# Performance work log

Hardware: AMD Instinct MI355X
Metric: run time of the kernel (lower is better)

The kernel has to match this reference:

```python
import jax, jax.numpy as jnp
import numpy as np

N = 2097152
RES = 512
N_LEVELS = 6  # 512,256,128,64,32,16 (stop at LIGHT_MIN_RES=16)
MIN_ROUGHNESS = 0.08
MAX_ROUGHNESS = 0.5


def _dot(a, b):
    return jnp.sum(a * b, axis=-1, keepdims=True)


def _safe_normalize(x):
    return x / jnp.sqrt(jnp.clip(_dot(x, x), 1e-20, None))


def _reflect(x, n):
    return 2.0 * _dot(x, n) * n - x


def _rgb_to_srgb(x):
    return jnp.where(x <= 0.0031308, 12.92 * x,
                     1.055 * jnp.power(jnp.maximum(x, 0.0031308), 1.0 / 2.4) - 0.055)


def _cube_face_uv(d):
    # OpenGL / nvdiffrast cube-map convention (inverse of util.cube_to_dir)
    x, y, z = d[..., 0], d[..., 1], d[..., 2]
    ax, ay, az = jnp.abs(x), jnp.abs(y), jnp.abs(z)
    is_x = (ax >= ay) & (ax >= az)
    is_y = (~is_x) & (ay >= az)
    face = jnp.where(is_x, jnp.where(x > 0, 0, 1),
           jnp.where(is_y, jnp.where(y > 0, 2, 3),
                           jnp.where(z > 0, 4, 5)))
    ma = jnp.maximum(jnp.where(is_x, ax, jnp.where(is_y, ay, az)), 1e-20)
    u = jnp.where(is_x, jnp.where(x > 0, -z, z),
        jnp.where(is_y, x, jnp.where(z > 0, x, -x)))
    v = jnp.where(is_y, jnp.where(y > 0, z, -z), -y)
    return face, u / ma, v / ma


def _bilinear_gather(tex, face, fx, fy):
    # tex: [6,H,W,C]; face/fx/fy: [N]
    H, W = tex.shape[1], tex.shape[2]
    x0 = jnp.floor(fx); y0 = jnp.floor(fy)
    tx = (fx - x0)[:, None]; ty = (fy - y0)[:, None]
    x0i = jnp.clip(x0.astype(jnp.int32), 0, W - 1)
    x1i = jnp.clip(x0i + 1, 0, W - 1)
    y0i = jnp.clip(y0.astype(jnp.int32), 0, H - 1)
    y1i = jnp.clip(y0i + 1, 0, H - 1)
    c00 = tex[face, y0i, x0i]; c01 = tex[face, y0i, x1i]
    c10 = tex[face, y1i, x0i]; c11 = tex[face, y1i, x1i]
    return (c00 * (1 - tx) + c01 * tx) * (1 - ty) + (c10 * (1 - tx) + c11 * tx) * ty


def _sample_cubemap(tex, dirs):
    H, W = tex.shape[1], tex.shape[2]
    face, u, v = _cube_face_uv(dirs)
    return _bilinear_gather(tex, face, (u * 0.5 + 0.5) * W - 0.5, (v * 0.5 + 0.5) * H - 0.5)


def _sample_cubemap_mip(mips, dirs, level):
    # trilinear: bilinear in each of the two bracketing mip levels + lerp on level
    L = len(mips)
    samples = jnp.stack([_sample_cubemap(m, dirs) for m in mips], axis=0)  # [L,N,C]
    lvl = jnp.clip(level, 0.0, L - 1.0)
    l0 = jnp.floor(lvl).astype(jnp.int32)
    l1 = jnp.minimum(l0 + 1, L - 1)
    f = (lvl - l0.astype(lvl.dtype))[:, None]
    n = jnp.arange(dirs.shape[0])
    return samples[l0, n] * (1 - f) + samples[l1, n] * f


def _sample_lut(lut, uv):
    # lut: [H,W,C]; uv in [0,1], u -> width, v -> height, clamp boundary
    H, W = lut.shape[0], lut.shape[1]
    fx = uv[:, 0] * W - 0.5; fy = uv[:, 1] * H - 0.5
    x0 = jnp.floor(fx); y0 = jnp.floor(fy)
    tx = (fx - x0)[:, None]; ty = (fy - y0)[:, None]
    x0i = jnp.clip(x0.astype(jnp.int32), 0, W - 1); x1i = jnp.clip(x0i + 1, 0, W - 1)
    y0i = jnp.clip(y0.astype(jnp.int32), 0, H - 1); y1i = jnp.clip(y0i + 1, 0, H - 1)
    c00 = lut[y0i, x0i]; c01 = lut[y0i, x1i]; c10 = lut[y1i, x0i]; c11 = lut[y1i, x1i]
    return (c00 * (1 - tx) + c01 * tx) * (1 - ty) + (c10 * (1 - tx) + c11 * tx) * ty


def _get_mip(roughness, n_levels):
    lo = (jnp.clip(roughness, MIN_ROUGHNESS, MAX_ROUGHNESS) - MIN_ROUGHNESS) \
         / (MAX_ROUGHNESS - MIN_ROUGHNESS) * (n_levels - 2)
    hi = (jnp.clip(roughness, MAX_ROUGHNESS, 1.0) - MAX_ROUGHNESS) / (1.0 - MAX_ROUGHNESS) + n_levels - 2
    return jnp.where(roughness < MAX_ROUGHNESS, lo, hi)


def _shade(view_dir, normal, kd, ks, reflect_occ, diffuse_map, mips, fg_lut):
    roughness = ks[:, 1:2]
    metallic = ks[:, 2:3]
    spec_col = (1.0 - metallic) * 0.04 + kd * metallic
    diff_col = kd * (1.0 - metallic)
    reflvec = _safe_normalize(_reflect(view_dir, normal))
    diffuse = jnp.clip(_sample_cubemap(diffuse_map, normal), 0.0, None)
    shaded = diffuse * diff_col * (1.0 - ks[:, 0:1])
    NdotV = jnp.clip(_dot(view_dir, normal), 1e-4, None)
    fg = _sample_lut(fg_lut, jnp.concatenate([NdotV, roughness], axis=-1))
    miplevel = _get_mip(roughness[:, 0], len(mips))
    spec = jnp.clip(_sample_cubemap_mip(mips, reflvec, miplevel), 0.0, None)
    reflectance = spec_col * fg[:, 0:1] + fg[:, 1:2]
    shaded = shaded + spec * reflectance * (1.0 - reflect_occ)
    return _rgb_to_srgb(jnp.clip(shaded, 0.0, 1.0))


def setup_inputs() -> dict:
    key = jax.random.key(0)
    k = jax.random.split(key, 16)
    inp = {
        "view_dir": _safe_normalize(jax.random.normal(k[0], (N, 3), jnp.float32)),
        "normal": _safe_normalize(jax.random.normal(k[1], (N, 3), jnp.float32)),
        "kd": jax.random.uniform(k[2], (N, 3), jnp.float32),
        "ks": jax.random.uniform(k[3], (N, 3), jnp.float32),
        "reflect_occ": jax.random.uniform(k[4], (N, 1), jnp.float32),
    }
    # learned / prefiltered environment light parameters (from build_mips)
    inp["diffuse_map"] = jax.random.uniform(k[5], (6, 16, 16, 3), jnp.float32)
    res = RES
    for i in range(N_LEVELS):
        inp[f"spec{i}"] = jax.random.uniform(k[6 + i], (6, res, res, 3), jnp.float32)
        res //= 2
    inp["fg_lut"] = jax.random.uniform(k[12], (256, 256, 2), jnp.float32)
    return inp


def reference(view_dir, normal, kd, ks, reflect_occ, diffuse_map,
              spec0, spec1, spec2, spec3, spec4, spec5, fg_lut):
    mips = [spec0, spec1, spec2, spec3, spec4, spec5]
    return _shade(view_dir, normal, kd, ks, reflect_occ, diffuse_map, mips, fg_lut)
```

## Files before the change

kernel.cpp:

```cpp
#include <hip/hip_runtime.h>
#include <math.h>


__device__ __forceinline__ void cube_face_uv(float x, float y, float z,
                                             int& face, float& uo, float& vo) {
    float ax = fabsf(x), ay = fabsf(y), az = fabsf(z);
    bool is_x = (ax >= ay) && (ax >= az);
    bool is_y = (!is_x) && (ay >= az);
    face = is_x ? (x > 0.f ? 0 : 1)
                : (is_y ? (y > 0.f ? 2 : 3) : (z > 0.f ? 4 : 5));
    float ma = fmaxf(is_x ? ax : (is_y ? ay : az), 1e-20f);
    float u = is_x ? (x > 0.f ? -z : z) : (is_y ? x : (z > 0.f ? x : -x));
    float v = is_y ? (y > 0.f ? z : -z) : -y;
    uo = u / ma;
    vo = v / ma;
}

__device__ __forceinline__ void bilinear3(const float* __restrict__ tex, int H, int W,
                                          int face, float fx, float fy,
                                          float& r, float& g, float& b) {
    float x0f = floorf(fx), y0f = floorf(fy);
    float tx = fx - x0f, ty = fy - y0f;
    int x0 = min(max((int)x0f, 0), W - 1);
    int x1 = min(x0 + 1, W - 1);
    int y0 = min(max((int)y0f, 0), H - 1);
    int y1 = min(y0 + 1, H - 1);
    const float* base = tex + (size_t)face * H * W * 3;
    const float* p00 = base + ((size_t)y0 * W + x0) * 3;
    const float* p01 = base + ((size_t)y0 * W + x1) * 3;
    const float* p10 = base + ((size_t)y1 * W + x0) * 3;
    const float* p11 = base + ((size_t)y1 * W + x1) * 3;
    float w00 = (1.f - tx) * (1.f - ty);
    float w01 = tx * (1.f - ty);
    float w10 = (1.f - tx) * ty;
    float w11 = tx * ty;
    r = p00[0] * w00 + p01[0] * w01 + p10[0] * w10 + p11[0] * w11;
    g = p00[1] * w00 + p01[1] * w01 + p10[1] * w10 + p11[1] * w11;
    b = p00[2] * w00 + p01[2] * w01 + p10[2] * w10 + p11[2] * w11;
}

__device__ __forceinline__ void sample_cubemap(const float* __restrict__ tex, int R,
                                               float dx, float dy, float dz,
                                               float& r, float& g, float& b) {
    int face; float u, v;
    cube_face_uv(dx, dy, dz, face, u, v);
    float fx = (u * 0.5f + 0.5f) * (float)R - 0.5f;
    float fy = (v * 0.5f + 0.5f) * (float)R - 0.5f;
    bilinear3(tex, R, R, face, fx, fy, r, g, b);
}

__device__ __forceinline__ void sample_lut2(const float* __restrict__ lut,
                                            float u, float v,
                                            float& o0, float& o1) {
    const int H = 256, W = 256;
    float fx = u * (float)W - 0.5f;
    float fy = v * (float)H - 0.5f;
    float x0f = floorf(fx), y0f = floorf(fy);
    float tx = fx - x0f, ty = fy - y0f;
    int x0 = min(max((int)x0f, 0), W - 1);
    int x1 = min(x0 + 1, W - 1);
    int y0 = min(max((int)y0f, 0), H - 1);
    int y1 = min(y0 + 1, H - 1);
    const float* p00 = lut + ((size_t)y0 * W + x0) * 2;
    const float* p01 = lut + ((size_t)y0 * W + x1) * 2;
    const float* p10 = lut + ((size_t)y1 * W + x0) * 2;
    const float* p11 = lut + ((size_t)y1 * W + x1) * 2;
    float w00 = (1.f - tx) * (1.f - ty);
    float w01 = tx * (1.f - ty);
    float w10 = (1.f - tx) * ty;
    float w11 = tx * ty;
    o0 = p00[0] * w00 + p01[0] * w01 + p10[0] * w10 + p11[0] * w11;
    o1 = p00[1] * w00 + p01[1] * w01 + p10[1] * w10 + p11[1] * w11;
}

__device__ __forceinline__ float rgb_to_srgb(float x) {
    return (x <= 0.0031308f) ? (12.92f * x)
                             : (1.055f * powf(fmaxf(x, 0.0031308f), 1.0f / 2.4f) - 0.055f);
}

__global__ __launch_bounds__(256)
void envlight_kernel(const float* __restrict__ view_dir,
                     const float* __restrict__ normal,
                     const float* __restrict__ kd,
                     const float* __restrict__ ks,
                     const float* __restrict__ reflect_occ,
                     const float* __restrict__ diffuse_map,
                     const float* __restrict__ s0, const float* __restrict__ s1,
                     const float* __restrict__ s2, const float* __restrict__ s3,
                     const float* __restrict__ s4, const float* __restrict__ s5,
                     const float* __restrict__ fg_lut,
                     float* __restrict__ out, int n)
{
    int i = blockIdx.x * blockDim.x + threadIdx.x;
    if (i >= n) return;

    float vx = view_dir[3 * i + 0], vy = view_dir[3 * i + 1], vz = view_dir[3 * i + 2];
    float nx = normal[3 * i + 0],  ny = normal[3 * i + 1],  nz = normal[3 * i + 2];
    float kdx = kd[3 * i + 0], kdy = kd[3 * i + 1], kdz = kd[3 * i + 2];
    float ks0 = ks[3 * i + 0], rough = ks[3 * i + 1], metallic = ks[3 * i + 2];
    float occ = reflect_occ[i];

    float scx = (1.f - metallic) * 0.04f + kdx * metallic;
    float scy = (1.f - metallic) * 0.04f + kdy * metallic;
    float scz = (1.f - metallic) * 0.04f + kdz * metallic;
    float dcx = kdx * (1.f - metallic);
    float dcy = kdy * (1.f - metallic);
    float dcz = kdz * (1.f - metallic);

    float vdotn = vx * nx + vy * ny + vz * nz;
    float rx = 2.f * vdotn * nx - vx;
    float ry = 2.f * vdotn * ny - vy;
    float rz = 2.f * vdotn * nz - vz;
    float rlen2 = fmaxf(rx * rx + ry * ry + rz * rz, 1e-20f);
    float rinv = rsqrtf(rlen2);
    rx *= rinv; ry *= rinv; rz *= rinv;

    float dfr, dfg, dfb;
    sample_cubemap(diffuse_map, 16, nx, ny, nz, dfr, dfg, dfb);
    dfr = fmaxf(dfr, 0.f); dfg = fmaxf(dfg, 0.f); dfb = fmaxf(dfb, 0.f);

    float shx = dfr * dcx * (1.f - ks0);
    float shy = dfg * dcy * (1.f - ks0);
    float shz = dfb * dcz * (1.f - ks0);

    float NdotV = fmaxf(vdotn, 1e-4f);
    float fg0, fg1;
    sample_lut2(fg_lut, NdotV, rough, fg0, fg1);

    const float MINR = 0.08f, MAXR = 0.5f;
    float lo = (fminf(fmaxf(rough, MINR), MAXR) - MINR) / (MAXR - MINR) * 4.0f;
    float hi = (fminf(fmaxf(rough, MAXR), 1.0f) - MAXR) / (1.0f - MAXR) + 4.0f;
    float lvl = (rough < MAXR) ? lo : hi;
    lvl = fminf(fmaxf(lvl, 0.f), 5.f);
    int l0 = (int)floorf(lvl);
    l0 = min(max(l0, 0), 5);
    int l1 = min(l0 + 1, 5);
    float f = lvl - (float)l0;

    const float* tA = (l0 == 0) ? s0 : (l0 == 1) ? s1 : (l0 == 2) ? s2
                     : (l0 == 3) ? s3 : (l0 == 4) ? s4 : s5;
    int RA = 512 >> l0;
    const float* tB = (l1 == 1) ? s1 : (l1 == 2) ? s2 : (l1 == 3) ? s3
                     : (l1 == 4) ? s4 : s5;
    int RB = 512 >> l1;

    float ar, ag, ab, br, bg, bb;
    sample_cubemap(tA, RA, rx, ry, rz, ar, ag, ab);
    sample_cubemap(tB, RB, rx, ry, rz, br, bg, bb);
    float spr = ar * (1.f - f) + br * f;
    float spg = ag * (1.f - f) + bg * f;
    float spb = ab * (1.f - f) + bb * f;
    spr = fmaxf(spr, 0.f); spg = fmaxf(spg, 0.f); spb = fmaxf(spb, 0.f);

    float rfx = scx * fg0 + fg1;
    float rfy = scy * fg0 + fg1;
    float rfz = scz * fg0 + fg1;

    float om = 1.f - occ;
    shx += spr * rfx * om;
    shy += spg * rfy * om;
    shz += spb * rfz * om;

    shx = fminf(fmaxf(shx, 0.f), 1.f);
    shy = fminf(fmaxf(shy, 0.f), 1.f);
    shz = fminf(fmaxf(shz, 0.f), 1.f);

    out[3 * i + 0] = rgb_to_srgb(shx);
    out[3 * i + 1] = rgb_to_srgb(shy);
    out[3 * i + 2] = rgb_to_srgb(shz);
}

extern "C" void kernel_launch(void* const* d_in, const int* in_sizes, int n_in,
                              void* d_out, int out_size, void* d_ws, size_t ws_size,
                              hipStream_t stream) {
    const float* view_dir    = (const float*)d_in[0];
    const float* normal      = (const float*)d_in[1];
    const float* kd          = (const float*)d_in[2];
    const float* ks          = (const float*)d_in[3];
    const float* reflect_occ = (const float*)d_in[4];
    const float* diffuse_map = (const float*)d_in[5];
    const float* s0          = (const float*)d_in[6];
    const float* s1          = (const float*)d_in[7];
    const float* s2          = (const float*)d_in[8];
    const float* s3          = (const float*)d_in[9];
    const float* s4          = (const float*)d_in[10];
    const float* s5          = (const float*)d_in[11];
    const float* fg_lut      = (const float*)d_in[12];
    float* out = (float*)d_out;

    int n = in_sizes[0] / 3;
    int block = 256;
    int grid = (n + block - 1) / block;
    envlight_kernel<<<grid, block, 0, stream>>>(view_dir, normal, kd, ks, reflect_occ,
                                                diffuse_map, s0, s1, s2, s3, s4, s5,
                                                fg_lut, out, n);
}
```

Baseline: 269.9 us.

## Process two points per thread with vectorized loads and batched gathers

Each thread now handles two consecutive points, reading inputs as float2 vectors and computing all bilinear addresses for both points before issuing any texture gathers, so more memory loads are in flight per thread. The mip pointer selection moves to a shared-memory table, and power-of-two shifts replace the multiplies in address math. Fast hardware intrinsics (rcp, rsq, exp2/log) replace the division and powf, and launch bounds request higher occupancy. In exchange, register pressure rises, and an odd n would make the second point read and write out of bounds.

```diff
diff --git a/kernel.cpp b/kernel.cpp
--- a/kernel.cpp
+++ b/kernel.cpp
@@ -2,83 +2,181 @@
 #include <math.h>
 
 
-__device__ __forceinline__ void cube_face_uv(float x, float y, float z,
-                                             int& face, float& uo, float& vo) {
-    float ax = fabsf(x), ay = fabsf(y), az = fabsf(z);
+struct BilinAddr {
+    int i00, i01, i10, i11;
+    float w00, w01, w10, w11;
+};
+
+__device__ __forceinline__ BilinAddr cube_addr(int lr, float dx, float dy, float dz) {
+    float ax = fabsf(dx), ay = fabsf(dy), az = fabsf(dz);
     bool is_x = (ax >= ay) && (ax >= az);
     bool is_y = (!is_x) && (ay >= az);
-    face = is_x ? (x > 0.f ? 0 : 1)
-                : (is_y ? (y > 0.f ? 2 : 3) : (z > 0.f ? 4 : 5));
+    int face = is_x ? (dx > 0.f ? 0 : 1)
+                    : (is_y ? (dy > 0.f ? 2 : 3) : (dz > 0.f ? 4 : 5));
     float ma = fmaxf(is_x ? ax : (is_y ? ay : az), 1e-20f);
-    float u = is_x ? (x > 0.f ? -z : z) : (is_y ? x : (z > 0.f ? x : -x));
-    float v = is_y ? (y > 0.f ? z : -z) : -y;
-    uo = u / ma;
-    vo = v / ma;
-}
-
-__device__ __forceinline__ void bilinear3(const float* __restrict__ tex, int H, int W,
-                                          int face, float fx, float fy,
-                                          float& r, float& g, float& b) {
+    float u = is_x ? (dx > 0.f ? -dz : dz) : (is_y ? dx : (dz > 0.f ? dx : -dx));
+    float v = is_y ? (dy > 0.f ? dz : -dz) : -dy;
+    float inv = __builtin_amdgcn_rcpf(ma);
+    float R = (float)(1 << lr);
+    float fx = (u * inv * 0.5f + 0.5f) * R - 0.5f;
+    float fy = (v * inv * 0.5f + 0.5f) * R - 0.5f;
     float x0f = floorf(fx), y0f = floorf(fy);
     float tx = fx - x0f, ty = fy - y0f;
+    int W = 1 << lr;
     int x0 = min(max((int)x0f, 0), W - 1);
     int x1 = min(x0 + 1, W - 1);
-    int y0 = min(max((int)y0f, 0), H - 1);
-    int y1 = min(y0 + 1, H - 1);
-    const float* base = tex + (size_t)face * H * W * 3;
-    const float* p00 = base + ((size_t)y0 * W + x0) * 3;
-    const float* p01 = base + ((size_t)y0 * W + x1) * 3;
-    const float* p10 = base + ((size_t)y1 * W + x0) * 3;
-    const float* p11 = base + ((size_t)y1 * W + x1) * 3;
-    float w00 = (1.f - tx) * (1.f - ty);
-    float w01 = tx * (1.f - ty);
-    float w10 = (1.f - tx) * ty;
-    float w11 = tx * ty;
-    r = p00[0] * w00 + p01[0] * w01 + p10[0] * w10 + p11[0] * w11;
-    g = p00[1] * w00 + p01[1] * w01 + p10[1] * w10 + p11[1] * w11;
-    b = p00[2] * w00 + p01[2] * w01 + p10[2] * w10 + p11[2] * w11;
-}
-
-__device__ __forceinline__ void sample_cubemap(const float* __restrict__ tex, int R,
-                                               float dx, float dy, float dz,
-                                               float& r, float& g, float& b) {
-    int face; float u, v;
-    cube_face_uv(dx, dy, dz, face, u, v);
-    float fx = (u * 0.5f + 0.5f) * (float)R - 0.5f;
-    float fy = (v * 0.5f + 0.5f) * (float)R - 0.5f;
-    bilinear3(tex, R, R, face, fx, fy, r, g, b);
-}
-
-__device__ __forceinline__ void sample_lut2(const float* __restrict__ lut,
-                                            float u, float v,
-                                            float& o0, float& o1) {
-    const int H = 256, W = 256;
-    float fx = u * (float)W - 0.5f;
-    float fy = v * (float)H - 0.5f;
-    float x0f = floorf(fx), y0f = floorf(fy);
-    float tx = fx - x0f, ty = fy - y0f;
-    int x0 = min(max((int)x0f, 0), W - 1);
-    int x1 = min(x0 + 1, W - 1);
-    int y0 = min(max((int)y0f, 0), H - 1);
-    int y1 = min(y0 + 1, H - 1);
-    const float* p00 = lut + ((size_t)y0 * W + x0) * 2;
-    const float* p01 = lut + ((size_t)y0 * W + x1) * 2;
-    const float* p10 = lut + ((size_t)y1 * W + x0) * 2;
-    const float* p11 = lut + ((size_t)y1 * W + x1) * 2;
-    float w00 = (1.f - tx) * (1.f - ty);
-    float w01 = tx * (1.f - ty);
-    float w10 = (1.f - tx) * ty;
-    float w11 = tx * ty;
-    o0 = p00[0] * w00 + p01[0] * w01 + p10[0] * w10 + p11[0] * w11;
-    o1 = p00[1] * w00 + p01[1] * w01 + p10[1] * w10 + p11[1] * w11;
-}
-
-__device__ __forceinline__ float rgb_to_srgb(float x) {
-    return (x <= 0.0031308f) ? (12.92f * x)
-                             : (1.055f * powf(fmaxf(x, 0.0031308f), 1.0f / 2.4f) - 0.055f);
-}
-
-__global__ __launch_bounds__(256)
+    int y0 = min(max((int)y0f, 0), W - 1);
+    int y1 = min(y0 + 1, W - 1);
+    int base = face << (2 * lr);
+    BilinAddr a;
+    a.i00 = (base + (y0 << lr) + x0) * 3;
+    a.i01 = (base + (y0 << lr) + x1) * 3;
+    a.i10 = (base + (y1 << lr) + x0) * 3;
+    a.i11 = (base + (y1 << lr) + x1) * 3;
+    a.w00 = (1.f - tx) * (1.f - ty);
+    a.w01 = tx * (1.f - ty);
+    a.w10 = (1.f - tx) * ty;
+    a.w11 = tx * ty;
+    return a;
+}
+
+__device__ __forceinline__ void gather3(const float* __restrict__ tex, const BilinAddr& a,
+                                        float& r, float& g, float& b) {
+    const float* p00 = tex + a.i00;
+    const float* p01 = tex + a.i01;
+    const float* p10 = tex + a.i10;
+    const float* p11 = tex + a.i11;
+    float c00x = p00[0], c00y = p00[1], c00z = p00[2];
+    float c01x = p01[0], c01y = p01[1], c01z = p01[2];
+    float c10x = p10[0], c10y = p10[1], c10z = p10[2];
+    float c11x = p11[0], c11y = p11[1], c11z = p11[2];
+    r = c00x * a.w00 + c01x * a.w01 + c10x * a.w10 + c11x * a.w11;
+    g = c00y * a.w00 + c01y * a.w01 + c10y * a.w10 + c11y * a.w11;
+    b = c00z * a.w00 + c01z * a.w01 + c10z * a.w10 + c11z * a.w11;
+}
+
+__device__ __forceinline__ float srgb1(float x) {
+    float p = 1.055f * __builtin_amdgcn_exp2f(
+                  __builtin_amdgcn_logf(fmaxf(x, 0.0031308f)) * (1.0f / 2.4f)) - 0.055f;
+    return (x <= 0.0031308f) ? (12.92f * x) : p;
+}
+
+struct PointCtx {
+    float vdotn;
+    float kdx, kdy, kdz;
+    float ks0, rough, metallic;
+    float occ;
+    BilinAddr aDiff;
+    BilinAddr aLut;
+    int lutI00, lutI01, lutI10, lutI11;
+    float lw00, lw01, lw10, lw11;
+    BilinAddr aA, aB;
+    const float* tA;
+    const float* tB;
+    float fmip;
+};
+
+__device__ __forceinline__ void point_setup(
+    float vx, float vy, float vz, float nx, float ny, float nz,
+    float kdx, float kdy, float kdz, float ks0, float rough, float metallic,
+    float occ, const float* const* mip_tbl, PointCtx& c)
+{
+    c.kdx = kdx; c.kdy = kdy; c.kdz = kdz;
+    c.ks0 = ks0; c.rough = rough; c.metallic = metallic; c.occ = occ;
+
+    float vdotn = vx * nx + vy * ny + vz * nz;
+    c.vdotn = vdotn;
+    float rx = 2.f * vdotn * nx - vx;
+    float ry = 2.f * vdotn * ny - vy;
+    float rz = 2.f * vdotn * nz - vz;
+    float rlen2 = fmaxf(rx * rx + ry * ry + rz * rz, 1e-20f);
+    float rinv = __builtin_amdgcn_rsqf(rlen2);
+    rx *= rinv; ry *= rinv; rz *= rinv;
+
+    c.aDiff = cube_addr(4, nx, ny, nz);
+
+    {
+        float NdotV = fmaxf(vdotn, 1e-4f);
+        float fx = NdotV * 256.f - 0.5f;
+        float fy = rough * 256.f - 0.5f;
+        float x0f = floorf(fx), y0f = floorf(fy);
+        float tx = fx - x0f, ty = fy - y0f;
+        int x0 = min(max((int)x0f, 0), 255);
+        int x1 = min(x0 + 1, 255);
+        int y0 = min(max((int)y0f, 0), 255);
+        int y1 = min(y0 + 1, 255);
+        c.lutI00 = y0 * 256 + x0;
+        c.lutI01 = y0 * 256 + x1;
+        c.lutI10 = y1 * 256 + x0;
+        c.lutI11 = y1 * 256 + x1;
+        c.lw00 = (1.f - tx) * (1.f - ty);
+        c.lw01 = tx * (1.f - ty);
+        c.lw10 = (1.f - tx) * ty;
+        c.lw11 = tx * ty;
+    }
+
+    const float MINR = 0.08f, MAXR = 0.5f;
+    float lo = (fminf(fmaxf(rough, MINR), MAXR) - MINR) * (4.0f / (MAXR - MINR));
+    float hi = (fminf(fmaxf(rough, MAXR), 1.0f) - MAXR) * (1.0f / (1.0f - MAXR)) + 4.0f;
+    float lvl = (rough < MAXR) ? lo : hi;
+    lvl = fminf(fmaxf(lvl, 0.f), 5.f);
+    int l0 = min(max((int)floorf(lvl), 0), 5);
+    int l1 = min(l0 + 1, 5);
+    c.fmip = lvl - (float)l0;
+    c.tA = mip_tbl[l0];
+    c.tB = mip_tbl[l1];
+    c.aA = cube_addr(9 - l0, rx, ry, rz);
+    c.aB = cube_addr(9 - l1, rx, ry, rz);
+}
+
+__device__ __forceinline__ void point_finish(
+    const PointCtx& c, const float* __restrict__ diffuse_map,
+    const float* __restrict__ fg_lut, float& o0, float& o1, float& o2)
+{
+    float dfr, dfg, dfb;
+    gather3(diffuse_map, c.aDiff, dfr, dfg, dfb);
+    dfr = fmaxf(dfr, 0.f); dfg = fmaxf(dfg, 0.f); dfb = fmaxf(dfb, 0.f);
+
+    const float2* lut2 = (const float2*)fg_lut;
+    float2 l00 = lut2[c.lutI00];
+    float2 l01 = lut2[c.lutI01];
+    float2 l10 = lut2[c.lutI10];
+    float2 l11 = lut2[c.lutI11];
+    float fg0 = l00.x * c.lw00 + l01.x * c.lw01 + l10.x * c.lw10 + l11.x * c.lw11;
+    float fg1 = l00.y * c.lw00 + l01.y * c.lw01 + l10.y * c.lw10 + l11.y * c.lw11;
+
+    float ar, ag, ab_, br, bg, bb;
+    gather3(c.tA, c.aA, ar, ag, ab_);
+    gather3(c.tB, c.aB, br, bg, bb);
+    float f = c.fmip;
+    float spr = fmaxf(ar * (1.f - f) + br * f, 0.f);
+    float spg = fmaxf(ag * (1.f - f) + bg * f, 0.f);
+    float spb = fmaxf(ab_ * (1.f - f) + bb * f, 0.f);
+
+    float m = c.metallic;
+    float scx = (1.f - m) * 0.04f + c.kdx * m;
+    float scy = (1.f - m) * 0.04f + c.kdy * m;
+    float scz = (1.f - m) * 0.04f + c.kdz * m;
+    float dcx = c.kdx * (1.f - m);
+    float dcy = c.kdy * (1.f - m);
+    float dcz = c.kdz * (1.f - m);
+
+    float kds = 1.f - c.ks0;
+    float shx = dfr * dcx * kds;
+    float shy = dfg * dcy * kds;
+    float shz = dfb * dcz * kds;
+
+    float om = 1.f - c.occ;
+    shx += spr * (scx * fg0 + fg1) * om;
+    shy += spg * (scy * fg0 + fg1) * om;
+    shz += spb * (scz * fg0 + fg1) * om;
+
+    o0 = srgb1(fminf(fmaxf(shx, 0.f), 1.f));
+    o1 = srgb1(fminf(fmaxf(shy, 0.f), 1.f));
+    o2 = srgb1(fminf(fmaxf(shz, 0.f), 1.f));
+}
+
+__global__ __launch_bounds__(256, 4)
 void envlight_kernel(const float* __restrict__ view_dir,
                      const float* __restrict__ normal,
                      const float* __restrict__ kd,
@@ -91,83 +189,42 @@
                      const float* __restrict__ fg_lut,
                      float* __restrict__ out, int n)
 {
-    int i = blockIdx.x * blockDim.x + threadIdx.x;
-    if (i >= n) return;
-
-    float vx = view_dir[3 * i + 0], vy = view_dir[3 * i + 1], vz = view_dir[3 * i + 2];
-    float nx = normal[3 * i + 0],  ny = normal[3 * i + 1],  nz = normal[3 * i + 2];
-    float kdx = kd[3 * i + 0], kdy = kd[3 * i + 1], kdz = kd[3 * i + 2];
-    float ks0 = ks[3 * i + 0], rough = ks[3 * i + 1], metallic = ks[3 * i + 2];
-    float occ = reflect_occ[i];
-
-    float scx = (1.f - metallic) * 0.04f + kdx * metallic;
-    float scy = (1.f - metallic) * 0.04f + kdy * metallic;
-    float scz = (1.f - metallic) * 0.04f + kdz * metallic;
-    float dcx = kdx * (1.f - metallic);
-    float dcy = kdy * (1.f - metallic);
-    float dcz = kdz * (1.f - metallic);
-
-    float vdotn = vx * nx + vy * ny + vz * nz;
-    float rx = 2.f * vdotn * nx - vx;
-    float ry = 2.f * vdotn * ny - vy;
-    float rz = 2.f * vdotn * nz - vz;
-    float rlen2 = fmaxf(rx * rx + ry * ry + rz * rz, 1e-20f);
-    float rinv = rsqrtf(rlen2);
-    rx *= rinv; ry *= rinv; rz *= rinv;
-
-    float dfr, dfg, dfb;
-    sample_cubemap(diffuse_map, 16, nx, ny, nz, dfr, dfg, dfb);
-    dfr = fmaxf(dfr, 0.f); dfg = fmaxf(dfg, 0.f); dfb = fmaxf(dfb, 0.f);
-
-    float shx = dfr * dcx * (1.f - ks0);
-    float shy = dfg * dcy * (1.f - ks0);
-    float shz = dfb * dcz * (1.f - ks0);
-
-    float NdotV = fmaxf(vdotn, 1e-4f);
-    float fg0, fg1;
-    sample_lut2(fg_lut, NdotV, rough, fg0, fg1);
-
-    const float MINR = 0.08f, MAXR = 0.5f;
-    float lo = (fminf(fmaxf(rough, MINR), MAXR) - MINR) / (MAXR - MINR) * 4.0f;
-    float hi = (fminf(fmaxf(rough, MAXR), 1.0f) - MAXR) / (1.0f - MAXR) + 4.0f;
-    float lvl = (rough < MAXR) ? lo : hi;
-    lvl = fminf(fmaxf(lvl, 0.f), 5.f);
-    int l0 = (int)floorf(lvl);
-    l0 = min(max(l0, 0), 5);
-    int l1 = min(l0 + 1, 5);
-    float f = lvl - (float)l0;
-
-    const float* tA = (l0 == 0) ? s0 : (l0 == 1) ? s1 : (l0 == 2) ? s2
-                     : (l0 == 3) ? s3 : (l0 == 4) ? s4 : s5;
-    int RA = 512 >> l0;
-    const float* tB = (l1 == 1) ? s1 : (l1 == 2) ? s2 : (l1 == 3) ? s3
-                     : (l1 == 4) ? s4 : s5;
-    int RB = 512 >> l1;
-
-    float ar, ag, ab, br, bg, bb;
-    sample_cubemap(tA, RA, rx, ry, rz, ar, ag, ab);
-    sample_cubemap(tB, RB, rx, ry, rz, br, bg, bb);
-    float spr = ar * (1.f - f) + br * f;
-    float spg = ag * (1.f - f) + bg * f;
-    float spb = ab * (1.f - f) + bb * f;
-    spr = fmaxf(spr, 0.f); spg = fmaxf(spg, 0.f); spb = fmaxf(spb, 0.f);
-
-    float rfx = scx * fg0 + fg1;
-    float rfy = scy * fg0 + fg1;
-    float rfz = scz * fg0 + fg1;
-
-    float om = 1.f - occ;
-    shx += spr * rfx * om;
-    shy += spg * rfy * om;
-    shz += spb * rfz * om;
-
-    shx = fminf(fmaxf(shx, 0.f), 1.f);
-    shy = fminf(fmaxf(shy, 0.f), 1.f);
-    shz = fminf(fmaxf(shz, 0.f), 1.f);
-
-    out[3 * i + 0] = rgb_to_srgb(shx);
-    out[3 * i + 1] = rgb_to_srgb(shy);
-    out[3 * i + 2] = rgb_to_srgb(shz);
+    __shared__ const float* mip_tbl[6];
+    if (threadIdx.x < 6) {
+        const float* p = (threadIdx.x == 0) ? s0 : (threadIdx.x == 1) ? s1
+                       : (threadIdx.x == 2) ? s2 : (threadIdx.x == 3) ? s3
+                       : (threadIdx.x == 4) ? s4 : s5;
+        mip_tbl[threadIdx.x] = p;
+    }
+    __syncthreads();
+
+    int t = blockIdx.x * blockDim.x + threadIdx.x;
+    int j = 2 * t;
+    if (j >= n) return;
+
+    const float2* v2 = (const float2*)view_dir;
+    const float2* n2 = (const float2*)normal;
+    const float2* k2 = (const float2*)kd;
+    const float2* q2 = (const float2*)ks;
+    float2 va = v2[3 * t], vb = v2[3 * t + 1], vc = v2[3 * t + 2];
+    float2 na = n2[3 * t], nb = n2[3 * t + 1], nc = n2[3 * t + 2];
+    float2 ka = k2[3 * t], kb = k2[3 * t + 1], kc = k2[3 * t + 2];
+    float2 qa = q2[3 * t], qb = q2[3 * t + 1], qc = q2[3 * t + 2];
+    float2 oc = ((const float2*)reflect_occ)[t];
+
+    PointCtx cA, cB;
+    point_setup(va.x, va.y, vb.x, na.x, na.y, nb.x,
+                ka.x, ka.y, kb.x, qa.x, qa.y, qb.x, oc.x, mip_tbl, cA);
+    point_setup(vb.y, vc.x, vc.y, nb.y, nc.x, nc.y,
+                kb.y, kc.x, kc.y, qb.y, qc.x, qc.y, oc.y, mip_tbl, cB);
+
+    float r0, g0, b0, r1, g1, b1;
+    point_finish(cA, diffuse_map, fg_lut, r0, g0, b0);
+    point_finish(cB, diffuse_map, fg_lut, r1, g1, b1);
+
+    float* o = out + 6 * (size_t)t;
+    o[0] = r0; o[1] = g0; o[2] = b0;
+    o[3] = r1; o[4] = g1; o[5] = b1;
 }
 
 extern "C" void kernel_launch(void* const* d_in, const int* in_sizes, int n_in,
@@ -189,8 +246,9 @@
     float* out = (float*)d_out;
 
     int n = in_sizes[0] / 3;
+    int nthreads = (n + 1) / 2;
     int block = 256;
-    int grid = (n + block - 1) / block;
+    int grid = (nthreads + block - 1) / block;
     envlight_kernel<<<grid, block, 0, stream>>>(view_dir, normal, kd, ks, reflect_occ,
                                                 diffuse_map, s0, s1, s2, s3, s4, s5,
                                                 fg_lut, out, n);
```

New measurement: 293.2 us. 1.09x slower.
